# Performance work log

Measured on AMD Instinct MI355X. Metric: run time of the kernel, lower is better.

The kernel has to match this reference:

```python
import jax, jax.numpy as jnp
import numpy as np

N_USERS = 400000
N_ITEMS = 200000
D = 64            # MAX_EMB_SIZE
N_LAYERS = 3
E = 600000        # user-item interactions; directed nnz = 2*E
B = 8192
N_NODES = N_USERS + N_ITEMS


def setup_inputs() -> dict:
    key = jax.random.key(0)
    ku, ki = jax.random.split(key)
    # nn.init.normal_(std=0.01)
    user_emb = 0.01 * jax.random.normal(ku, (N_USERS, D), dtype=jnp.float32)
    item_emb = 0.01 * jax.random.normal(ki, (N_ITEMS, D), dtype=jnp.float32)

    rng = np.random.default_rng(0)
    # per-row embedding sizes -> prefix masks (mask[r, :sizes[r]] = 1)
    user_sizes = rng.integers(1, D + 1, size=N_USERS)
    item_sizes = rng.integers(1, D + 1, size=N_ITEMS)
    ar = np.arange(D)[None, :]
    user_mask = (ar < user_sizes[:, None]).astype(np.int32)
    item_mask = (ar < item_sizes[:, None]).astype(np.int32)

    # symmetric normalized bipartite adjacency (D^-1/2 A D^-1/2), COO
    u = rng.integers(0, N_USERS, size=E)
    it = rng.integers(0, N_ITEMS, size=E) + N_USERS
    rows = np.concatenate([u, it]).astype(np.int32)
    cols = np.concatenate([it, u]).astype(np.int32)
    deg = np.bincount(rows, minlength=N_NODES).astype(np.float64)
    dinv = np.where(deg > 0, 1.0 / np.sqrt(np.maximum(deg, 1.0)), 0.0)
    vals = (dinv[rows] * dinv[cols]).astype(np.float32)

    users = rng.integers(0, N_USERS, size=B).astype(np.int32)
    pos_items = rng.integers(0, N_ITEMS, size=B).astype(np.int32)
    neg_items = rng.integers(0, N_ITEMS, size=B).astype(np.int32)

    return {
        "user_emb": user_emb,
        "item_emb": item_emb,
        "user_mask": jnp.asarray(user_mask),
        "item_mask": jnp.asarray(item_mask),
        "adj_row": jnp.asarray(rows),
        "adj_col": jnp.asarray(cols),
        "adj_val": jnp.asarray(vals),
        "users": jnp.asarray(users),
        "pos_items": jnp.asarray(pos_items),
        "neg_items": jnp.asarray(neg_items),
    }


def reference(user_emb, item_emb, user_mask, item_mask,
              adj_row, adj_col, adj_val, users, pos_items, neg_items):
    um = user_mask.astype(user_emb.dtype)
    im = item_mask.astype(item_emb.dtype)

    def spmm(x):  # [N_NODES, D] -> [N_NODES, D]
        msgs = adj_val[:, None] * x[adj_col]
        return jax.ops.segment_sum(msgs, adj_row, num_segments=N_NODES)

    all_emb = jnp.concatenate([user_emb * um, item_emb * im], axis=0)
    acc = all_emb  # running sum over layers (mean at the end)
    x = all_emb
    for _ in range(N_LAYERS):
        x = spmm(x)
        acc = acc + x
    light_out = acc / (N_LAYERS + 1)

    users_emb = light_out[users]
    pos_emb = light_out[N_USERS + pos_items]
    neg_emb = light_out[N_USERS + neg_items]
    users_emb_ego = user_emb[users] * um[users]
    pos_emb_ego = item_emb[pos_items] * im[pos_items]
    neg_emb_ego = item_emb[neg_items] * im[neg_items]
    return (users_emb, pos_emb, neg_emb, users_emb_ego, pos_emb_ego, neg_emb_ego)
```

## Files before the change

### kernel.cpp

```cpp
#include <hip/hip_runtime.h>

#define N_USERS 400000
#define N_ITEMS 200000
#define NNODES  600000
#define D 64
#define B 8192
#define NBKT 8

typedef int v4i __attribute__((ext_vector_type(4)));

__device__ __forceinline__ float bflo(unsigned u) { return __uint_as_float(u << 16); }
__device__ __forceinline__ float bfhi(unsigned u) { return __uint_as_float(u & 0xffff0000u); }
__device__ __forceinline__ unsigned f2bf(float f) {
    unsigned u = __float_as_uint(f);
    unsigned r = u + 0x7fffu + ((u >> 16) & 1u);
    return r >> 16;
}

__device__ __forceinline__ void unpack_fma(float* acc, uint4 wv, float v) {
    acc[0] += v * bflo(wv.x); acc[1] += v * bfhi(wv.x);
    acc[2] += v * bflo(wv.y); acc[3] += v * bfhi(wv.y);
    acc[4] += v * bflo(wv.z); acc[5] += v * bfhi(wv.z);
    acc[6] += v * bflo(wv.w); acc[7] += v * bfhi(wv.w);
}

__device__ __forceinline__ int bucket_of(int r) {
    return (r < N_USERS) ? (r / 100000) : (4 + (r - N_USERS) / 50000);
}

__global__ void k_hrs(const int* __restrict__ rows, int* __restrict__ deg,
                      int* __restrict__ rank,
                      const int* __restrict__ users, const int* __restrict__ pos,
                      const int* __restrict__ neg,
                      char* __restrict__ flag1, char* __restrict__ flag2,
                      int nnz, int nhist) {
    int bid = blockIdx.x;
    int t = threadIdx.x;
    if (bid < nhist) {
        int x = bid & 7;
        int e = (bid >> 3) * 256 + t;
        if (e >= nnz) return;
        int r = rows[e];
        if (bucket_of(r) == x) rank[e] = atomicAdd(&deg[r], 1);
    } else {
        int slot2 = (bid - nhist) * 256 + t;
        if (slot2 >= 3 * B) return;
        int set = slot2 / B;
        int b = slot2 - set * B;
        int r;
        if (set == 0)      r = users[b];
        else if (set == 1) r = N_USERS + pos[b];
        else               r = N_USERS + neg[b];
        flag2[r] = 1;
        flag1[r] = 1;
    }
}

__global__ void k_scan1(int* __restrict__ deg, int* __restrict__ sums,
                        float* __restrict__ dinv, int n) {
    __shared__ int lds[256];
    int i = blockIdx.x * 256 + threadIdx.x;
    int v = (i < n) ? deg[i] : 0;
    if (i < n) dinv[i] = (v > 0) ? (float)(1.0 / sqrt((double)v)) : 0.0f;
    lds[threadIdx.x] = v;
    __syncthreads();
    for (int off = 1; off < 256; off <<= 1) {
        int t = (threadIdx.x >= off) ? lds[threadIdx.x - off] : 0;
        __syncthreads();
        lds[threadIdx.x] += t;
        __syncthreads();
    }
    int inc = lds[threadIdx.x];
    if (i < n) deg[i] = inc - v;
    if (threadIdx.x == 255) sums[blockIdx.x] = inc;
}

__global__ void k_scan2(int* __restrict__ sums, int n) {
    __shared__ int lds[1024];
    __shared__ int carry;
    if (threadIdx.x == 0) carry = 0;
    __syncthreads();
    for (int base = 0; base < n; base += 1024) {
        int i = base + threadIdx.x;
        int v = (i < n) ? sums[i] : 0;
        lds[threadIdx.x] = v;
        __syncthreads();
        for (int off = 1; off < 1024; off <<= 1) {
            int t = (threadIdx.x >= off) ? lds[threadIdx.x - off] : 0;
            __syncthreads();
            lds[threadIdx.x] += t;
            __syncthreads();
        }
        int inc = lds[threadIdx.x];
        if (i < n) sums[i] = (inc - v) + carry;
        __syncthreads();
        if (threadIdx.x == 1023) carry += lds[1023];
        __syncthreads();
    }
}

__global__ void k_scan3p1(const int* __restrict__ deg, const int* __restrict__ sums,
                          int* __restrict__ row_ptr,
                          const int* __restrict__ rows, const int* __restrict__ cols,
                          char* __restrict__ flag2, int nnz, int scan_blocks) {
    int bid = blockIdx.x;
    int t = threadIdx.x;
    if (bid < scan_blocks) {
        int i = bid * 256 + t;
        if (i >= NNODES) return;
        row_ptr[i] = deg[i] + sums[i >> 8];
        if (i == 0) row_ptr[NNODES] = nnz;
    } else {
        int e = (bid - scan_blocks) * 256 + t;
        if (e >= nnz) return;
        if (flag2[rows[e]]) flag2[cols[e]] = 1;
    }
}

__global__ void k_fatS(const int* __restrict__ rows, const int* __restrict__ cols,
                       const int* __restrict__ rank, const int* __restrict__ row_ptr,
                       int* __restrict__ pcol,
                       const int* __restrict__ um, const int* __restrict__ im,
                       int* __restrict__ sizes, int nnz) {
    int bid = blockIdx.x;
    int x = bid & 7;
    int g = bid >> 3;
    int st = g / 12;
    int slot = g - st * 12;
    int t = threadIdx.x;
    if (slot < 8) {
        int e = (st * 8 + slot) * 256 + t;
        if (e >= nnz) return;
        int r = rows[e];
        if (bucket_of(r) != x) return;
        pcol[row_ptr[r] + rank[e]] = cols[e];
    } else {
        int sb = (st * 4 + (slot - 8)) * 8 + x;
        int r = sb * 32 + (t >> 3);
        int q = t & 7;
        if (r >= NNODES) return;
        const v4i* p = (const v4i*)((r < N_USERS) ? um + (size_t)r * D
                                                  : im + (size_t)(r - N_USERS) * D);
        v4i v0 = __builtin_nontemporal_load(p + q);
        v4i v1 = __builtin_nontemporal_load(p + 8 + q);
        int s = v0[0] + v0[1] + v0[2] + v0[3] + v1[0] + v1[1] + v1[2] + v1[3];
        s += __shfl_xor(s, 1);
        s += __shfl_xor(s, 2);
        s += __shfl_xor(s, 4);
        if (q == 0) sizes[r] = s;
    }
}

__global__ void k_pass2(const int* __restrict__ rows, const int* __restrict__ cols,
                        const char* __restrict__ flag2, char* __restrict__ flag1,
                        int* __restrict__ cnt2, int nnz, int eb) {
    int bid = blockIdx.x;
    int t = threadIdx.x;
    if (bid < eb) {
        int base = bid * 1024 + t;
        int r4[4], c4[4];
        #pragma unroll
        for (int k = 0; k < 4; ++k) {
            int e = base + k * 256;
            r4[k] = (e < nnz) ? rows[e] : -1;
            c4[k] = (e < nnz) ? cols[e] : 0;
        }
        char f4[4];
        #pragma unroll
        for (int k = 0; k < 4; ++k) f4[k] = (r4[k] >= 0) ? flag2[r4[k]] : (char)0;
        #pragma unroll
        for (int k = 0; k < 4; ++k) if (f4[k]) flag1[c4[k]] = 1;
        return;
    }
    int tb = bid - eb;
    int r = tb * 256 + t;
    char f = (r < NNODES) ? flag2[r] : 0;
    if (f) flag1[r] = 1;
    unsigned long long bal = __ballot(f != 0);
    __shared__ int ws[4];
    int lane = t & 63, wv = t >> 6;
    if (lane == 0) ws[wv] = (int)__popcll(bal);
    __syncthreads();
    if (t == 0) cnt2[tb] = ws[0] + ws[1] + ws[2] + ws[3];
}

__global__ void k_cnt1(const char* __restrict__ flag1, int* __restrict__ cnt1) {
    int tb = blockIdx.x;
    int t = threadIdx.x;
    int r = tb * 256 + t;
    char f = (r < NNODES) ? flag1[r] : 0;
    unsigned long long bal = __ballot(f != 0);
    __shared__ int ws[4];
    int lane = t & 63, wv = t >> 6;
    if (lane == 0) ws[wv] = (int)__popcll(bal);
    __syncthreads();
    if (t == 0) cnt1[tb] = ws[0] + ws[1] + ws[2] + ws[3];
}

__global__ void k_scan_dual(int* __restrict__ a, int* __restrict__ b, int n,
                            int* __restrict__ totA, int* __restrict__ totB) {
    __shared__ int lds[1024];
    __shared__ int carry;
    for (int pass = 0; pass < 2; ++pass) {
        int* arr = pass ? b : a;
        if (threadIdx.x == 0) carry = 0;
        __syncthreads();
        for (int base = 0; base < n; base += 1024) {
            int i = base + threadIdx.x;
            int v = (i < n) ? arr[i] : 0;
            lds[threadIdx.x] = v;
            __syncthreads();
            for (int off = 1; off < 1024; off <<= 1) {
                int t = (threadIdx.x >= off) ? lds[threadIdx.x - off] : 0;
                __syncthreads();
                lds[threadIdx.x] += t;
                __syncthreads();
            }
            int inc = lds[threadIdx.x];
            if (i < n) arr[i] = (inc - v) + carry;
            __syncthreads();
            if (threadIdx.x == 1023) carry += lds[1023];
            __syncthreads();
        }
        if (threadIdx.x == 0) { if (pass) *totB = carry; else *totA = carry; }
        __syncthreads();
    }
}

__global__ void k_fill(const char* __restrict__ flag1, const char* __restrict__ flag2,
                       const int* __restrict__ cnt1, const int* __restrict__ cnt2,
                       int* __restrict__ wl1, int* __restrict__ wl2) {
    int tb = blockIdx.x;
    int t = threadIdx.x;
    int r = tb * 256 + t;
    bool a = (r < NNODES) && flag1[r];
    bool b = (r < NNODES) && flag2[r];
    int lane = t & 63, wv = t >> 6;
    unsigned long long lt = (1ull << lane) - 1ull;
    unsigned long long ba = __ballot(a);
    unsigned long long bb = __ballot(b);
    __shared__ int wa[4], wb[4];
    if (lane == 0) { wa[wv] = (int)__popcll(ba); wb[wv] = (int)__popcll(bb); }
    __syncthreads();
    int offA = 0, offB = 0;
    for (int i = 0; i < wv; ++i) { offA += wa[i]; offB += wb[i]; }
    if (a) wl1[cnt1[tb] + offA + (int)__popcll(ba & lt)] = r;
    if (b) wl2[cnt2[tb] + offB + (int)__popcll(bb & lt)] = r;
}

__global__ void k_spmm1(const int* __restrict__ row_ptr, const int* __restrict__ pcol,
                        const float* __restrict__ dinv, const int* __restrict__ sizes,
                        const int* __restrict__ wl1, const int* __restrict__ wl1_cnt,
                        const float* __restrict__ ue, const float* __restrict__ ie,
                        unsigned* __restrict__ y1) {
    int tid = blockIdx.x * blockDim.x + threadIdx.x;
    int w = tid >> 3;
    if (w >= *wl1_cnt) return;
    int r = wl1[w];
    int c8 = (tid & 7) << 3;
    int s = row_ptr[r];
    int e = row_ptr[r + 1];
    float dr = dinv[r];
    float acc[8] = {0.f, 0.f, 0.f, 0.f, 0.f, 0.f, 0.f, 0.f};
    int i = s;
    for (; i + 1 < e; i += 2) {
        int c0 = pcol[i], c1 = pcol[i + 1];
        float v0 = dr * dinv[c0], v1 = dr * dinv[c1];
        int sz0 = sizes[c0], sz1 = sizes[c1];
        const float* p0 = ((c0 < N_USERS) ? ue + (size_t)c0 * D
                                          : ie + (size_t)(c0 - N_USERS) * D) + c8;
        const float* p1 = ((c1 < N_USERS) ? ue + (size_t)c1 * D
                                          : ie + (size_t)(c1 - N_USERS) * D) + c8;
        float4 a0 = *(const float4*)p0;
        float4 a1 = *(const float4*)(p0 + 4);
        float4 b0 = *(const float4*)p1;
        float4 b1 = *(const float4*)(p1 + 4);
        acc[0] += v0 * ((c8 + 0 < sz0) ? a0.x : 0.f) + v1 * ((c8 + 0 < sz1) ? b0.x : 0.f);
        acc[1] += v0 * ((c8 + 1 < sz0) ? a0.y : 0.f) + v1 * ((c8 + 1 < sz1) ? b0.y : 0.f);
        acc[2] += v0 * ((c8 + 2 < sz0) ? a0.z : 0.f) + v1 * ((c8 + 2 < sz1) ? b0.z : 0.f);
        acc[3] += v0 * ((c8 + 3 < sz0) ? a0.w : 0.f) + v1 * ((c8 + 3 < sz1) ? b0.w : 0.f);
        acc[4] += v0 * ((c8 + 4 < sz0) ? a1.x : 0.f) + v1 * ((c8 + 4 < sz1) ? b1.x : 0.f);
        acc[5] += v0 * ((c8 + 5 < sz0) ? a1.y : 0.f) + v1 * ((c8 + 5 < sz1) ? b1.y : 0.f);
        acc[6] += v0 * ((c8 + 6 < sz0) ? a1.z : 0.f) + v1 * ((c8 + 6 < sz1) ? b1.z : 0.f);
        acc[7] += v0 * ((c8 + 7 < sz0) ? a1.w : 0.f) + v1 * ((c8 + 7 < sz1) ? b1.w : 0.f);
    }
    if (i < e) {
        int c = pcol[i];
        float v = dr * dinv[c];
        int sz = sizes[c];
        const float* p = ((c < N_USERS) ? ue + (size_t)c * D
                                        : ie + (size_t)(c - N_USERS) * D) + c8;
        float4 e0 = *(const float4*)p;
        float4 e1 = *(const float4*)(p + 4);
        acc[0] += v * ((c8 + 0 < sz) ? e0.x : 0.f);
        acc[1] += v * ((c8 + 1 < sz) ? e0.y : 0.f);
        acc[2] += v * ((c8 + 2 < sz) ? e0.z : 0.f);
        acc[3] += v * ((c8 + 3 < sz) ? e0.w : 0.f);
        acc[4] += v * ((c8 + 4 < sz) ? e1.x : 0.f);
        acc[5] += v * ((c8 + 5 < sz) ? e1.y : 0.f);
        acc[6] += v * ((c8 + 6 < sz) ? e1.z : 0.f);
        acc[7] += v * ((c8 + 7 < sz) ? e1.w : 0.f);
    }
    uint4 o;
    o.x = f2bf(acc[0]) | (f2bf(acc[1]) << 16);
    o.y = f2bf(acc[2]) | (f2bf(acc[3]) << 16);
    o.z = f2bf(acc[4]) | (f2bf(acc[5]) << 16);
    o.w = f2bf(acc[6]) | (f2bf(acc[7]) << 16);
    *(uint4*)(y1 + (size_t)r * 32 + (tid & 7) * 4) = o;
}

__global__ void k_spmm2(const int* __restrict__ row_ptr, const int* __restrict__ pcol,
                        const float* __restrict__ dinv,
                        const int* __restrict__ wl2, const int* __restrict__ wl2_cnt,
                        const unsigned* __restrict__ y1, unsigned* __restrict__ x2) {
    int tid = blockIdx.x * blockDim.x + threadIdx.x;
    int w = tid >> 3;
    if (w >= *wl2_cnt) return;
    int r = wl2[w];
    int cp = (tid & 7) << 2;
    int s = row_ptr[r];
    int e = row_ptr[r + 1];
    float dr = dinv[r];
    float acc[8] = {0.f, 0.f, 0.f, 0.f, 0.f, 0.f, 0.f, 0.f};
    int i = s;
    for (; i + 1 < e; i += 2) {
        int c0 = pcol[i], c1 = pcol[i + 1];
        float v0 = dr * dinv[c0], v1 = dr * dinv[c1];
        uint4 w0 = *(const uint4*)(y1 + (size_t)c0 * 32 + cp);
        uint4 w1 = *(const uint4*)(y1 + (size_t)c1 * 32 + cp);
        unpack_fma(acc, w0, v0);
        unpack_fma(acc, w1, v1);
    }
    if (i < e) {
        int c0 = pcol[i];
        float v0 = dr * dinv[c0];
        uint4 w0 = *(const uint4*)(y1 + (size_t)c0 * 32 + cp);
        unpack_fma(acc, w0, v0);
    }
    uint4 o;
    o.x = f2bf(acc[0]) | (f2bf(acc[1]) << 16);
    o.y = f2bf(acc[2]) | (f2bf(acc[3]) << 16);
    o.z = f2bf(acc[4]) | (f2bf(acc[5]) << 16);
    o.w = f2bf(acc[6]) | (f2bf(acc[7]) << 16);
    *(uint4*)(x2 + (size_t)r * 32 + cp) = o;
}

__global__ void k_spmm3(const int* __restrict__ row_ptr, const int* __restrict__ pcol,
                        const float* __restrict__ dinv, const int* __restrict__ sizes,
                        const float* __restrict__ ue, const float* __restrict__ ie,
                        const unsigned* __restrict__ y1, const unsigned* __restrict__ x2,
                        const int* __restrict__ users, const int* __restrict__ pos,
                        const int* __restrict__ neg, float* __restrict__ out) {
    int tid = blockIdx.x * blockDim.x + threadIdx.x;
    int slot = tid >> 3;
    if (slot >= 3 * B) return;
    int cp = (tid & 7) << 2;
    int c8 = (tid & 7) << 3;
    int set = slot / B;
    int b = slot - set * B;
    int r;
    if (set == 0)      r = users[b];
    else if (set == 1) r = N_USERS + pos[b];
    else               r = N_USERS + neg[b];
    int s = row_ptr[r];
    int e = row_ptr[r + 1];
    float dr = dinv[r];
    float acc[8] = {0.f, 0.f, 0.f, 0.f, 0.f, 0.f, 0.f, 0.f};
    uint4 g1 = *(const uint4*)(y1 + (size_t)r * 32 + cp);
    uint4 g2 = *(const uint4*)(x2 + (size_t)r * 32 + cp);
    unpack_fma(acc, g1, 1.0f);
    unpack_fma(acc, g2, 1.0f);
    int i = s;
    for (; i + 1 < e; i += 2) {
        int c0 = pcol[i], c1 = pcol[i + 1];
        float v0 = dr * dinv[c0], v1 = dr * dinv[c1];
        uint4 w0 = *(const uint4*)(x2 + (size_t)c0 * 32 + cp);
        uint4 w1 = *(const uint4*)(x2 + (size_t)c1 * 32 + cp);
        unpack_fma(acc, w0, v0);
        unpack_fma(acc, w1, v1);
    }
    if (i < e) {
        int c0 = pcol[i];
        float v0 = dr * dinv[c0];
        uint4 w0 = *(const uint4*)(x2 + (size_t)c0 * 32 + cp);
        unpack_fma(acc, w0, v0);
    }
    const float* p = ((r < N_USERS) ? ue + (size_t)r * D
                                    : ie + (size_t)(r - N_USERS) * D) + c8;
    float4 e0 = *(const float4*)p;
    float4 e1 = *(const float4*)(p + 4);
    int sz = sizes[r];
    e0.x = (c8 + 0 < sz) ? e0.x : 0.f; e0.y = (c8 + 1 < sz) ? e0.y : 0.f;
    e0.z = (c8 + 2 < sz) ? e0.z : 0.f; e0.w = (c8 + 3 < sz) ? e0.w : 0.f;
    e1.x = (c8 + 4 < sz) ? e1.x : 0.f; e1.y = (c8 + 5 < sz) ? e1.y : 0.f;
    e1.z = (c8 + 6 < sz) ? e1.z : 0.f; e1.w = (c8 + 7 < sz) ? e1.w : 0.f;
    float4 oa, ob;
    oa.x = (e0.x + acc[0]) * 0.25f; oa.y = (e0.y + acc[1]) * 0.25f;
    oa.z = (e0.z + acc[2]) * 0.25f; oa.w = (e0.w + acc[3]) * 0.25f;
    ob.x = (e1.x + acc[4]) * 0.25f; ob.y = (e1.y + acc[5]) * 0.25f;
    ob.z = (e1.z + acc[6]) * 0.25f; ob.w = (e1.w + acc[7]) * 0.25f;
    float* o0 = out + (size_t)slot * D + c8;
    float* o1 = out + (size_t)(3 * B + slot) * D + c8;
    *(float4*)o0 = oa; *(float4*)(o0 + 4) = ob;
    *(float4*)o1 = e0; *(float4*)(o1 + 4) = e1;
}

extern "C" void kernel_launch(void* const* d_in, const int* in_sizes, int n_in,
                              void* d_out, int out_size, void* d_ws, size_t ws_size,
                              hipStream_t stream) {
    const float* ue   = (const float*)d_in[0];
    const float* ie   = (const float*)d_in[1];
    const int*   um   = (const int*)d_in[2];
    const int*   im   = (const int*)d_in[3];
    const int*   rows = (const int*)d_in[4];
    const int*   cols = (const int*)d_in[5];
    const int*   users = (const int*)d_in[7];
    const int*   pos   = (const int*)d_in[8];
    const int*   neg   = (const int*)d_in[9];
    int nnz = in_sizes[4];

    float* out = (float*)d_out;

    unsigned short* Y1 = (unsigned short*)d_ws;
    unsigned short* X2 = Y1 + (size_t)NNODES * D;
    int*   deg     = (int*)(X2 + (size_t)NNODES * D);
    int*   row_ptr = deg + NNODES;
    int*   sizes   = row_ptr + NNODES + 1;
    int*   sums    = sizes + NNODES;
    int*   wcnt    = sums + 4096;
    int*   cnt1    = wcnt + 16;
    int*   cnt2    = cnt1 + 2360;
    float* dinv    = (float*)(cnt2 + 2360);
    int*   pcol    = (int*)(dinv + NNODES);
    char*  flag1   = (char*)(pcol + nnz);
    char*  flag2   = flag1 + NNODES;
    int*   wl1     = (int*)(((uintptr_t)(flag2 + NNODES) + 15) & ~(uintptr_t)15);
    int*   wl2     = wl1 + NNODES;
    int*   rank    = wl2 + NNODES;

    const int blk = 256;
    const int scan_blocks = (NNODES + 255) / 256;
    int chunks = (nnz + 255) / 256;
    int nst = (chunks + 7) / 8;
    int nhist = chunks * 8;
    int seed_blocks = (3 * B + blk - 1) / blk;

    hipMemsetAsync(deg, 0, (size_t)NNODES * sizeof(int), stream);
    hipMemsetAsync(flag1, 0, (size_t)2 * NNODES, stream);

    k_hrs<<<nhist + seed_blocks, blk, 0, stream>>>(rows, deg, rank,
                                                   users, pos, neg,
                                                   flag1, flag2, nnz, nhist);

    k_scan1<<<scan_blocks, 256, 0, stream>>>(deg, sums, dinv, NNODES);
    k_scan2<<<1, 1024, 0, stream>>>(sums, scan_blocks);
    k_scan3p1<<<scan_blocks + chunks, blk, 0, stream>>>(deg, sums, row_ptr,
                                                        rows, cols, flag2,
                                                        nnz, scan_blocks);

    k_fatS<<<nst * 12 * 8, blk, 0, stream>>>(rows, cols, rank, row_ptr, pcol,
                                             um, im, sizes, nnz);

    {
        int eb = (nnz + 1023) / 1024;
        k_pass2<<<eb + scan_blocks, blk, 0, stream>>>(rows, cols, flag2, flag1,
                                                      cnt2, nnz, eb);
    }

    k_cnt1<<<scan_blocks, blk, 0, stream>>>(flag1, cnt1);
    k_scan_dual<<<1, 1024, 0, stream>>>(cnt1, cnt2, scan_blocks, wcnt, wcnt + 1);
    k_fill<<<scan_blocks, blk, 0, stream>>>(flag1, flag2, cnt1, cnt2, wl1, wl2);

    int n_full = NNODES * 8;
    int n_samp = 3 * B * 8;

    k_spmm1<<<(n_full + blk - 1) / blk, blk, 0, stream>>>(row_ptr, pcol, dinv, sizes,
                                                          wl1, wcnt,
                                                          ue, ie, (unsigned*)Y1);
    k_spmm2<<<(n_full + blk - 1) / blk, blk, 0, stream>>>(row_ptr, pcol, dinv,
                                                          wl2, wcnt + 1,
                                                          (const unsigned*)Y1, (unsigned*)X2);
    k_spmm3<<<(n_samp + blk - 1) / blk, blk, 0, stream>>>(row_ptr, pcol, dinv, sizes,
                                                          ue, ie,
                                                          (const unsigned*)Y1,
                                                          (const unsigned*)X2,
                                                          users, pos, neg, out);
}
```

Before: 215.6 us.

## Merge frontier-expansion passes into scan kernels to cut kernel launches

Moves the first frontier-expansion pass (flag2 propagation) into the first scan kernel, moves the second pass (flag1 marking plus cnt2 counting) into the row_ptr finalize kernel, and moves the cnt1 counting into the CSR fill kernel. This removes two launches and the serialization gaps between them. It depends on those passes not needing each other's outputs. The cnt1 count in k_fatS reads flag1 after k_s3p2 has finished, so ordering still holds.

```diff
diff --git a/kernel.cpp b/kernel.cpp
--- a/kernel.cpp
+++ b/kernel.cpp
@@ -56,23 +56,43 @@
     }
 }
 
-__global__ void k_scan1(int* __restrict__ deg, int* __restrict__ sums,
-                        float* __restrict__ dinv, int n) {
-    __shared__ int lds[256];
-    int i = blockIdx.x * 256 + threadIdx.x;
-    int v = (i < n) ? deg[i] : 0;
-    if (i < n) dinv[i] = (v > 0) ? (float)(1.0 / sqrt((double)v)) : 0.0f;
-    lds[threadIdx.x] = v;
-    __syncthreads();
-    for (int off = 1; off < 256; off <<= 1) {
-        int t = (threadIdx.x >= off) ? lds[threadIdx.x - off] : 0;
-        __syncthreads();
-        lds[threadIdx.x] += t;
-        __syncthreads();
-    }
-    int inc = lds[threadIdx.x];
-    if (i < n) deg[i] = inc - v;
-    if (threadIdx.x == 255) sums[blockIdx.x] = inc;
+__global__ void k_s1p1(int* __restrict__ deg, int* __restrict__ sums,
+                       float* __restrict__ dinv,
+                       const int* __restrict__ rows, const int* __restrict__ cols,
+                       char* __restrict__ flag2, int nnz, int scan_blocks) {
+    int bid = blockIdx.x;
+    int t = threadIdx.x;
+    if (bid < scan_blocks) {
+        __shared__ int lds[256];
+        int i = bid * 256 + t;
+        int v = (i < NNODES) ? deg[i] : 0;
+        if (i < NNODES) dinv[i] = (v > 0) ? (float)(1.0 / sqrt((double)v)) : 0.0f;
+        lds[t] = v;
+        __syncthreads();
+        for (int off = 1; off < 256; off <<= 1) {
+            int tv = (t >= off) ? lds[t - off] : 0;
+            __syncthreads();
+            lds[t] += tv;
+            __syncthreads();
+        }
+        int inc = lds[t];
+        if (i < NNODES) deg[i] = inc - v;
+        if (t == 255) sums[bid] = inc;
+    } else {
+        int base = (bid - scan_blocks) * 1024 + t;
+        int r4[4], c4[4];
+        #pragma unroll
+        for (int k = 0; k < 4; ++k) {
+            int e = base + k * 256;
+            r4[k] = (e < nnz) ? rows[e] : -1;
+            c4[k] = (e < nnz) ? cols[e] : 0;
+        }
+        char f4[4];
+        #pragma unroll
+        for (int k = 0; k < 4; ++k) f4[k] = (r4[k] >= 0) ? flag2[r4[k]] : (char)0;
+        #pragma unroll
+        for (int k = 0; k < 4; ++k) if (f4[k]) flag2[c4[k]] = 1;
+    }
 }
 
 __global__ void k_scan2(int* __restrict__ sums, int n) {
@@ -99,10 +119,11 @@
     }
 }
 
-__global__ void k_scan3p1(const int* __restrict__ deg, const int* __restrict__ sums,
-                          int* __restrict__ row_ptr,
-                          const int* __restrict__ rows, const int* __restrict__ cols,
-                          char* __restrict__ flag2, int nnz, int scan_blocks) {
+__global__ void k_s3p2(const int* __restrict__ deg, const int* __restrict__ sums,
+                       int* __restrict__ row_ptr,
+                       const int* __restrict__ rows, const int* __restrict__ cols,
+                       const char* __restrict__ flag2, char* __restrict__ flag1,
+                       int* __restrict__ cnt2, int nnz, int scan_blocks, int eb) {
     int bid = blockIdx.x;
     int t = threadIdx.x;
     if (bid < scan_blocks) {
@@ -110,10 +131,31 @@
         if (i >= NNODES) return;
         row_ptr[i] = deg[i] + sums[i >> 8];
         if (i == 0) row_ptr[NNODES] = nnz;
+    } else if (bid < scan_blocks + eb) {
+        int base = (bid - scan_blocks) * 1024 + t;
+        int r4[4], c4[4];
+        #pragma unroll
+        for (int k = 0; k < 4; ++k) {
+            int e = base + k * 256;
+            r4[k] = (e < nnz) ? rows[e] : -1;
+            c4[k] = (e < nnz) ? cols[e] : 0;
+        }
+        char f4[4];
+        #pragma unroll
+        for (int k = 0; k < 4; ++k) f4[k] = (r4[k] >= 0) ? flag2[r4[k]] : (char)0;
+        #pragma unroll
+        for (int k = 0; k < 4; ++k) if (f4[k]) flag1[c4[k]] = 1;
     } else {
-        int e = (bid - scan_blocks) * 256 + t;
-        if (e >= nnz) return;
-        if (flag2[rows[e]]) flag2[cols[e]] = 1;
+        int tb = bid - scan_blocks - eb;
+        int r = tb * 256 + t;
+        char f = (r < NNODES) ? flag2[r] : 0;
+        if (f) flag1[r] = 1;
+        unsigned long long bal = __ballot(f != 0);
+        __shared__ int ws[4];
+        int lane = t & 63, wv = t >> 6;
+        if (lane == 0) ws[wv] = (int)__popcll(bal);
+        __syncthreads();
+        if (t == 0) cnt2[tb] = ws[0] + ws[1] + ws[2] + ws[3];
     }
 }
 
@@ -121,13 +163,27 @@
                        const int* __restrict__ rank, const int* __restrict__ row_ptr,
                        int* __restrict__ pcol,
                        const int* __restrict__ um, const int* __restrict__ im,
-                       int* __restrict__ sizes, int nnz) {
+                       int* __restrict__ sizes,
+                       const char* __restrict__ flag1, int* __restrict__ cnt1,
+                       int nnz, int nsc) {
     int bid = blockIdx.x;
+    int t = threadIdx.x;
+    if (bid >= nsc) {
+        int tb = bid - nsc;
+        int r = tb * 256 + t;
+        char f = (r < NNODES) ? flag1[r] : 0;
+        unsigned long long bal = __ballot(f != 0);
+        __shared__ int ws[4];
+        int lane = t & 63, wv = t >> 6;
+        if (lane == 0) ws[wv] = (int)__popcll(bal);
+        __syncthreads();
+        if (t == 0) cnt1[tb] = ws[0] + ws[1] + ws[2] + ws[3];
+        return;
+    }
     int x = bid & 7;
     int g = bid >> 3;
     int st = g / 12;
     int slot = g - st * 12;
-    int t = threadIdx.x;
     if (slot < 8) {
         int e = (st * 8 + slot) * 256 + t;
         if (e >= nnz) return;
@@ -149,52 +205,6 @@
         s += __shfl_xor(s, 4);
         if (q == 0) sizes[r] = s;
     }
-}
-
-__global__ void k_pass2(const int* __restrict__ rows, const int* __restrict__ cols,
-                        const char* __restrict__ flag2, char* __restrict__ flag1,
-                        int* __restrict__ cnt2, int nnz, int eb) {
-    int bid = blockIdx.x;
-    int t = threadIdx.x;
-    if (bid < eb) {
-        int base = bid * 1024 + t;
-        int r4[4], c4[4];
-        #pragma unroll
-        for (int k = 0; k < 4; ++k) {
-            int e = base + k * 256;
-            r4[k] = (e < nnz) ? rows[e] : -1;
-            c4[k] = (e < nnz) ? cols[e] : 0;
-        }
-        char f4[4];
-        #pragma unroll
-        for (int k = 0; k < 4; ++k) f4[k] = (r4[k] >= 0) ? flag2[r4[k]] : (char)0;
-        #pragma unroll
-        for (int k = 0; k < 4; ++k) if (f4[k]) flag1[c4[k]] = 1;
-        return;
-    }
-    int tb = bid - eb;
-    int r = tb * 256 + t;
-    char f = (r < NNODES) ? flag2[r] : 0;
-    if (f) flag1[r] = 1;
-    unsigned long long bal = __ballot(f != 0);
-    __shared__ int ws[4];
-    int lane = t & 63, wv = t >> 6;
-    if (lane == 0) ws[wv] = (int)__popcll(bal);
-    __syncthreads();
-    if (t == 0) cnt2[tb] = ws[0] + ws[1] + ws[2] + ws[3];
-}
-
-__global__ void k_cnt1(const char* __restrict__ flag1, int* __restrict__ cnt1) {
-    int tb = blockIdx.x;
-    int t = threadIdx.x;
-    int r = tb * 256 + t;
-    char f = (r < NNODES) ? flag1[r] : 0;
-    unsigned long long bal = __ballot(f != 0);
-    __shared__ int ws[4];
-    int lane = t & 63, wv = t >> 6;
-    if (lane == 0) ws[wv] = (int)__popcll(bal);
-    __syncthreads();
-    if (t == 0) cnt1[tb] = ws[0] + ws[1] + ws[2] + ws[3];
 }
 
 __global__ void k_scan_dual(int* __restrict__ a, int* __restrict__ b, int n,
@@ -444,6 +454,8 @@
     int nst = (chunks + 7) / 8;
     int nhist = chunks * 8;
     int seed_blocks = (3 * B + blk - 1) / blk;
+    int eb = (nnz + 1023) / 1024;
+    int nsc = nst * 12 * 8;
 
     hipMemsetAsync(deg, 0, (size_t)NNODES * sizeof(int), stream);
     hipMemsetAsync(flag1, 0, (size_t)2 * NNODES, stream);
@@ -452,22 +464,18 @@
                                                    users, pos, neg,
                                                    flag1, flag2, nnz, nhist);
 
-    k_scan1<<<scan_blocks, 256, 0, stream>>>(deg, sums, dinv, NNODES);
+    k_s1p1<<<scan_blocks + eb, blk, 0, stream>>>(deg, sums, dinv,
+                                                 rows, cols, flag2, nnz, scan_blocks);
+
     k_scan2<<<1, 1024, 0, stream>>>(sums, scan_blocks);
-    k_scan3p1<<<scan_blocks + chunks, blk, 0, stream>>>(deg, sums, row_ptr,
-                                                        rows, cols, flag2,
-                                                        nnz, scan_blocks);
-
-    k_fatS<<<nst * 12 * 8, blk, 0, stream>>>(rows, cols, rank, row_ptr, pcol,
-                                             um, im, sizes, nnz);
-
-    {
-        int eb = (nnz + 1023) / 1024;
-        k_pass2<<<eb + scan_blocks, blk, 0, stream>>>(rows, cols, flag2, flag1,
-                                                      cnt2, nnz, eb);
-    }
-
-    k_cnt1<<<scan_blocks, blk, 0, stream>>>(flag1, cnt1);
+
+    k_s3p2<<<scan_blocks + eb + scan_blocks, blk, 0, stream>>>(
+        deg, sums, row_ptr, rows, cols, flag2, flag1, cnt2, nnz, scan_blocks, eb);
+
+    k_fatS<<<nsc + scan_blocks, blk, 0, stream>>>(rows, cols, rank, row_ptr, pcol,
+                                                  um, im, sizes, flag1, cnt1,
+                                                  nnz, nsc);
+
     k_scan_dual<<<1, 1024, 0, stream>>>(cnt1, cnt2, scan_blocks, wcnt, wcnt + 1);
     k_fill<<<scan_blocks, blk, 0, stream>>>(flag1, flag2, cnt1, cnt2, wl1, wl2);
 
```

New measurement: 211.5 us. No clear change (-1.9%).
